# Optimization experiments

Measured on AMD Instinct MI355X. Metric: run time of the kernel, lower is better.

Reference implementation:

```python
import jax, jax.numpy as jnp
import numpy as np

N, T, D, M = 16, 4096, 256, 512


def setup_inputs() -> dict:
    key = jax.random.key(0)
    k1, k2 = jax.random.split(key)
    x = jax.random.normal(k1, (N, T, D), dtype=jnp.float32)
    # codebook initialized like the module: uniform(-1/M, 1/M) then row-normalized
    init_bound = 1.0 / M
    emb = jax.random.uniform(k2, (M, D), dtype=jnp.float32, minval=-init_bound, maxval=init_bound)
    emb = emb / (jnp.linalg.norm(emb, axis=1, keepdims=True) + 1e-4)
    return {"x": x, "embedding": emb}


def reference(x, embedding):
    sg = jax.lax.stop_gradient
    # L2_distance: distances computed against the row-normalized codebook,
    # but the gather uses the raw (unnormalized) codebook.
    emb_norm = embedding / (jnp.linalg.norm(embedding, axis=1, keepdims=True) + 1e-4)
    x_flat = sg(x).reshape(-1, D)  # (N*T, D), detached in torch
    distances = (jnp.sum(emb_norm ** 2, axis=1)[None, :]
                 + jnp.sum(x_flat ** 2, axis=1, keepdims=True)
                 - 2.0 * (x_flat @ emb_norm.T))  # (N*T, M)
    indices = jnp.argmin(distances, axis=-1)  # (N*T,)
    encodings = jax.nn.one_hot(indices, M, dtype=jnp.float32)  # (N*T, M)
    quantized = embedding[indices].reshape(x.shape)  # (N, T, D)

    commitment_loss = jnp.mean((sg(x) - quantized) ** 2)
    quantized_ = x + sg(quantized - x)           # straight-through
    quantized_ = (quantized_ + quantized) / 2.0  # averaged with raw-grad path

    avg_probs = jnp.mean(encodings, axis=0)  # (M,)
    perplexity = jnp.exp(-jnp.sum(avg_probs * jnp.log(avg_probs + 1e-10)))
    return quantized_, commitment_loss, perplexity
```

## Files before the change

### kernel.cpp

```cpp
#include <hip/hip_runtime.h>
#include <hip/hip_bf16.h>


typedef _Float16 half8_t __attribute__((ext_vector_type(8)));
typedef _Float16 half4_t __attribute__((ext_vector_type(4)));
typedef float f32x4 __attribute__((ext_vector_type(4)));

static constexpr int kRows = 65536;
static constexpr int kD = 256;
static constexpr int kM = 512;

typedef const unsigned int __attribute__((address_space(1)))* gas_t;
typedef unsigned int __attribute__((address_space(3)))* las_t;

__global__ void vq_prep(const float* __restrict__ emb, _Float16* __restrict__ swz,
                        float* __restrict__ bias, unsigned int* __restrict__ hist,
                        float* __restrict__ loss) {
    const int j = blockIdx.x;
    const int lane = threadIdx.x;
    float4 v = ((const float4*)(emb + j * kD))[lane];
    float ss = v.x * v.x + v.y * v.y + v.z * v.z + v.w * v.w;
    #pragma unroll
    for (int off = 32; off > 0; off >>= 1) ss += __shfl_xor(ss, off);
    const float scale = 1.0f / (sqrtf(ss) + 1e-4f);
    if (lane == 0) bias[j] = 0.5f * ss * scale * scale;
    half4_t h;
    h[0] = (_Float16)(v.x * scale);
    h[1] = (_Float16)(v.y * scale);
    h[2] = (_Float16)(v.z * scale);
    h[3] = (_Float16)(v.w * scale);
    const int k0 = lane * 4;
    const int ko = k0 >> 5;
    const int qd = (k0 >> 3) & 3;
    const int jj = k0 & 7;
    const int off_h = (j >> 4) * 4096 + ko * 512 + (qd * 16 + (j & 15)) * 8 + jj;
    *(half4_t*)(swz + off_h) = h;
    if (j == 0) {
        for (int b = lane; b < kM; b += 64) hist[b] = 0u;
        if (lane == 0) loss[0] = 0.0f;
    }
}

__global__ __launch_bounds__(128, 2) void vq_argmin(
    const float* __restrict__ x, const _Float16* __restrict__ bswz,
    const float* __restrict__ bias, unsigned int* __restrict__ hist,
    int* __restrict__ idx_out) {
    __shared__ _Float16 bb[2][32 * kD];
    __shared__ float lbias[kM];
    __shared__ unsigned int lhist[kM];

    const int t = threadIdx.x;
    const int row0 = blockIdx.x * 64;
    const int wave = t >> 6;
    const int lane = t & 63;
    const int qd = lane >> 4;
    const int ln = lane & 15;

    #pragma unroll
    for (int b = t; b < kM; b += 128) { lhist[b] = 0u; lbias[b] = bias[b]; }

    half8_t a[2][8];
    #pragma unroll
    for (int s = 0; s < 2; ++s) {
        const float* xr = x + (size_t)(row0 + wave * 32 + s * 16 + ln) * kD + qd * 8;
        #pragma unroll
        for (int ko = 0; ko < 8; ++ko) {
            const float4 v0 = *(const float4*)(xr + ko * 32);
            const float4 v1 = *(const float4*)(xr + ko * 32 + 4);
            half8_t h;
            h[0] = (_Float16)v0.x; h[1] = (_Float16)v0.y;
            h[2] = (_Float16)v0.z; h[3] = (_Float16)v0.w;
            h[4] = (_Float16)v1.x; h[5] = (_Float16)v1.y;
            h[6] = (_Float16)v1.z; h[7] = (_Float16)v1.w;
            a[s][ko] = h;
        }
    }

    auto stage_load = [&](int st, int buf) {
        const _Float16* src = bswz + (size_t)st * 8192 + t * 8;
        _Float16* dst = &bb[buf][0] + t * 8;
        #pragma unroll
        for (int i = 0; i < 8; ++i)
            __builtin_amdgcn_global_load_lds((gas_t)(const void*)(src + i * 1024),
                                             (las_t)(void*)(dst + i * 1024), 16, 0, 0);
    };

    stage_load(0, 0);

    float bv[2][4] = {{-1e30f, -1e30f, -1e30f, -1e30f}, {-1e30f, -1e30f, -1e30f, -1e30f}};
    int bi[2][4] = {{0, 0, 0, 0}, {0, 0, 0, 0}};
    #pragma unroll 1
    for (int st = 0; st < 16; ++st) {
        if (st < 15) stage_load(st + 1, (st + 1) & 1);
        if (st == 0)       __asm__ __volatile__("s_waitcnt vmcnt(8) lgkmcnt(0)\ns_barrier" ::: "memory");
        else if (st < 15)  __asm__ __volatile__("s_waitcnt vmcnt(8)\ns_barrier" ::: "memory");
        else               __asm__ __volatile__("s_waitcnt vmcnt(0)\ns_barrier" ::: "memory");

        const _Float16* bbase = &bb[st & 1][0];
        #pragma unroll
        for (int sg = 0; sg < 2; ++sg) {
            const int c = st * 32 + sg * 16 + ln;
            const float bbias = lbias[c];
            f32x4 acc0 = {-bbias, -bbias, -bbias, -bbias};
            f32x4 acc1 = {-bbias, -bbias, -bbias, -bbias};
            const half8_t* bp = (const half8_t*)bbase + sg * 512 + lane;
            #pragma unroll
            for (int ko = 0; ko < 8; ++ko) {
                const half8_t bf = bp[ko * 64];
                acc0 = __builtin_amdgcn_mfma_f32_16x16x32_f16(a[0][ko], bf, acc0, 0, 0, 0);
                acc1 = __builtin_amdgcn_mfma_f32_16x16x32_f16(a[1][ko], bf, acc1, 0, 0, 0);
            }
            #pragma unroll
            for (int r = 0; r < 4; ++r) {
                if (acc0[r] > bv[0][r]) { bv[0][r] = acc0[r]; bi[0][r] = c; }
                if (acc1[r] > bv[1][r]) { bv[1][r] = acc1[r]; bi[1][r] = c; }
            }
        }
        if (st < 15) __asm__ __volatile__("s_barrier" ::: "memory");
    }

    #pragma unroll
    for (int s = 0; s < 2; ++s) {
        #pragma unroll
        for (int r = 0; r < 4; ++r) {
            #pragma unroll
            for (int off = 1; off < 16; off <<= 1) {
                const float ov = __shfl_xor(bv[s][r], off);
                const int oi = __shfl_xor(bi[s][r], off);
                if (ov > bv[s][r] || (ov == bv[s][r] && oi < bi[s][r])) { bv[s][r] = ov; bi[s][r] = oi; }
            }
            if (ln == 0) {
                idx_out[row0 + wave * 32 + s * 16 + qd * 4 + r] = bi[s][r];
                atomicAdd(&lhist[bi[s][r]], 1u);
            }
        }
    }
    __syncthreads();

    #pragma unroll
    for (int b = t; b < kM; b += 128) {
        const unsigned int h = lhist[b];
        if (h) atomicAdd(&hist[b], h);
    }
}

__global__ __launch_bounds__(256) void vq_epilogue(
    const float* __restrict__ x, const float* __restrict__ emb,
    const int* __restrict__ idx, float* __restrict__ loss_accum,
    float* __restrict__ out) {
    __shared__ int li[64];
    __shared__ float lred[4];
    const int t = threadIdx.x;
    const int row0 = blockIdx.x * 64;
    if (t < 64) li[t] = idx[row0 + t];
    __syncthreads();

    float lsum = 0.0f;
    const float* xg = x + (size_t)row0 * kD;
    float* og = out + (size_t)row0 * kD;
    #pragma unroll
    for (int i = 0; i < 16; ++i) {
        const int g = t * 4 + i * 1024;
        const int r = g >> 8;
        const float4 xv = *(const float4*)(xg + g);
        const float4 q = *(const float4*)(emb + (size_t)li[r] * kD + (g & 255));
        const float d0 = xv.x - q.x, d1 = xv.y - q.y, d2 = xv.z - q.z, d3 = xv.w - q.w;
        lsum += d0 * d0 + d1 * d1 + d2 * d2 + d3 * d3;
        float4 o;
        o.x = ((xv.x + (q.x - xv.x)) + q.x) * 0.5f;
        o.y = ((xv.y + (q.y - xv.y)) + q.y) * 0.5f;
        o.z = ((xv.z + (q.z - xv.z)) + q.z) * 0.5f;
        o.w = ((xv.w + (q.w - xv.w)) + q.w) * 0.5f;
        *(float4*)&og[g] = o;
    }
    #pragma unroll
    for (int off = 32; off > 0; off >>= 1) lsum += __shfl_xor(lsum, off);
    if ((t & 63) == 0) lred[t >> 6] = lsum;
    __syncthreads();
    if (t == 0) atomicAdd(loss_accum, lred[0] + lred[1] + lred[2] + lred[3]);
}

__global__ void vq_final(const unsigned int* __restrict__ hist,
                         const float* __restrict__ loss_accum,
                         float* __restrict__ out) {
    const int t = threadIdx.x;
    __shared__ float sr[4];
    float s = 0.0f;
    for (int b = t; b < kM; b += 256) {
        const float p = (float)hist[b] * (1.0f / 65536.0f);
        s += p * logf(p + 1e-10f);
    }
    #pragma unroll
    for (int off = 32; off > 0; off >>= 1) s += __shfl_xor(s, off);
    if ((t & 63) == 0) sr[t >> 6] = s;
    __syncthreads();
    if (t == 0) {
        const float tot = sr[0] + sr[1] + sr[2] + sr[3];
        out[16777217] = expf(-tot);
        out[16777216] = loss_accum[0] * (1.0f / 16777216.0f);
    }
}

extern "C" void kernel_launch(void* const* d_in, const int* in_sizes, int n_in,
                              void* d_out, int out_size, void* d_ws, size_t ws_size,
                              hipStream_t stream) {
    const float* x = (const float*)d_in[0];
    const float* emb = (const float*)d_in[1];
    char* ws = (char*)d_ws;
    _Float16* bswz = (_Float16*)ws;
    float* bias = (float*)(ws + 262144);
    unsigned int* hist = (unsigned int*)(ws + 262144 + 2048);
    float* loss = (float*)(ws + 262144 + 4096);
    int* idx = (int*)(ws + 262144 + 4096 + 64);
    float* out = (float*)d_out;

    vq_prep<<<kM, 64, 0, stream>>>(emb, bswz, bias, hist, loss);
    vq_argmin<<<kRows / 64, 128, 0, stream>>>(x, bswz, bias, hist, idx);
    vq_epilogue<<<kRows / 64, 256, 0, stream>>>(x, emb, idx, loss, out);
    vq_final<<<1, 256, 0, stream>>>(hist, loss, out);
}
```

Measured before the change: 167.4 us.

## Keep codebook fragments in registers and stage x tile in LDS for argmin

Restructures the argmin kernel so each of 8 waves holds a 64-code slice of the fp16 codebook in registers, while a 128-row x tile is converted to fp16 and stored in padded LDS. Scores are offset by 64 so they stay positive, then packed with the code index into a uint so that argmax becomes an integer max. Per-wave winners are reduced across waves through shared memory. This removes the per-stage codebook streaming and barriers, at the cost of heavy register use (64 half8 B fragments) and precision lost by truncating low mantissa bits, which may change tie-breaking on near-equal distances.

```diff
diff --git a/kernel.cpp b/kernel.cpp
--- a/kernel.cpp
+++ b/kernel.cpp
@@ -9,9 +9,7 @@
 static constexpr int kRows = 65536;
 static constexpr int kD = 256;
 static constexpr int kM = 512;
-
-typedef const unsigned int __attribute__((address_space(1)))* gas_t;
-typedef unsigned int __attribute__((address_space(3)))* las_t;
+static constexpr int kSH = 264;
 
 __global__ void vq_prep(const float* __restrict__ emb, _Float16* __restrict__ swz,
                         float* __restrict__ bias, unsigned int* __restrict__ hist,
@@ -41,106 +39,106 @@
     }
 }
 
-__global__ __launch_bounds__(128, 2) void vq_argmin(
+__global__ __launch_bounds__(512, 2) void vq_argmin(
     const float* __restrict__ x, const _Float16* __restrict__ bswz,
     const float* __restrict__ bias, unsigned int* __restrict__ hist,
     int* __restrict__ idx_out) {
-    __shared__ _Float16 bb[2][32 * kD];
-    __shared__ float lbias[kM];
+    __shared__ _Float16 xs[2][64 * kSH];
+    __shared__ unsigned int red[8 * 128];
     __shared__ unsigned int lhist[kM];
 
     const int t = threadIdx.x;
-    const int row0 = blockIdx.x * 64;
+    const int row0 = blockIdx.x * 128;
     const int wave = t >> 6;
     const int lane = t & 63;
     const int qd = lane >> 4;
     const int ln = lane & 15;
 
-    #pragma unroll
-    for (int b = t; b < kM; b += 128) { lhist[b] = 0u; lbias[b] = bias[b]; }
-
-    half8_t a[2][8];
-    #pragma unroll
-    for (int s = 0; s < 2; ++s) {
-        const float* xr = x + (size_t)(row0 + wave * 32 + s * 16 + ln) * kD + qd * 8;
-        #pragma unroll
-        for (int ko = 0; ko < 8; ++ko) {
-            const float4 v0 = *(const float4*)(xr + ko * 32);
-            const float4 v1 = *(const float4*)(xr + ko * 32 + 4);
+    lhist[t] = 0u;
+
+    half8_t bfrag[4][8];
+    #pragma unroll
+    for (int nt = 0; nt < 4; ++nt)
+        #pragma unroll
+        for (int ko = 0; ko < 8; ++ko)
+            bfrag[nt][ko] = *(const half8_t*)(bswz + (size_t)(wave * 4 + nt) * 4096 + ko * 512 + lane * 8);
+
+    float binit[4];
+    #pragma unroll
+    for (int nt = 0; nt < 4; ++nt) binit[nt] = 64.0f - bias[wave * 64 + nt * 16 + ln];
+
+    {
+        const float* xg = x + (size_t)row0 * kD;
+        #pragma unroll
+        for (int i = 0; i < 8; ++i) {
+            const int fi = t * 8 + i * 4096;
+            const float4 v0 = *(const float4*)(xg + fi);
+            const float4 v1 = *(const float4*)(xg + fi + 4);
+            const int r = fi >> 8, c = fi & 255;
             half8_t h;
             h[0] = (_Float16)v0.x; h[1] = (_Float16)v0.y;
             h[2] = (_Float16)v0.z; h[3] = (_Float16)v0.w;
             h[4] = (_Float16)v1.x; h[5] = (_Float16)v1.y;
             h[6] = (_Float16)v1.z; h[7] = (_Float16)v1.w;
-            a[s][ko] = h;
+            *(half8_t*)&xs[r >> 6][(r & 63) * kSH + c] = h;
         }
     }
-
-    auto stage_load = [&](int st, int buf) {
-        const _Float16* src = bswz + (size_t)st * 8192 + t * 8;
-        _Float16* dst = &bb[buf][0] + t * 8;
-        #pragma unroll
-        for (int i = 0; i < 8; ++i)
-            __builtin_amdgcn_global_load_lds((gas_t)(const void*)(src + i * 1024),
-                                             (las_t)(void*)(dst + i * 1024), 16, 0, 0);
-    };
-
-    stage_load(0, 0);
-
-    float bv[2][4] = {{-1e30f, -1e30f, -1e30f, -1e30f}, {-1e30f, -1e30f, -1e30f, -1e30f}};
-    int bi[2][4] = {{0, 0, 0, 0}, {0, 0, 0, 0}};
+    __syncthreads();
+
     #pragma unroll 1
-    for (int st = 0; st < 16; ++st) {
-        if (st < 15) stage_load(st + 1, (st + 1) & 1);
-        if (st == 0)       __asm__ __volatile__("s_waitcnt vmcnt(8) lgkmcnt(0)\ns_barrier" ::: "memory");
-        else if (st < 15)  __asm__ __volatile__("s_waitcnt vmcnt(8)\ns_barrier" ::: "memory");
-        else               __asm__ __volatile__("s_waitcnt vmcnt(0)\ns_barrier" ::: "memory");
-
-        const _Float16* bbase = &bb[st & 1][0];
-        #pragma unroll
-        for (int sg = 0; sg < 2; ++sg) {
-            const int c = st * 32 + sg * 16 + ln;
-            const float bbias = lbias[c];
-            f32x4 acc0 = {-bbias, -bbias, -bbias, -bbias};
-            f32x4 acc1 = {-bbias, -bbias, -bbias, -bbias};
-            const half8_t* bp = (const half8_t*)bbase + sg * 512 + lane;
+    for (int tile = 0; tile < 2; ++tile) {
+        const _Float16* xb = &xs[tile][0];
+        #pragma unroll
+        for (int mt = 0; mt < 4; ++mt) {
+            half8_t a[8];
             #pragma unroll
-            for (int ko = 0; ko < 8; ++ko) {
-                const half8_t bf = bp[ko * 64];
-                acc0 = __builtin_amdgcn_mfma_f32_16x16x32_f16(a[0][ko], bf, acc0, 0, 0, 0);
-                acc1 = __builtin_amdgcn_mfma_f32_16x16x32_f16(a[1][ko], bf, acc1, 0, 0, 0);
+            for (int ko = 0; ko < 8; ++ko)
+                a[ko] = *(const half8_t*)(xb + (mt * 16 + ln) * kSH + qd * 8 + ko * 32);
+            unsigned int best[4] = {0u, 0u, 0u, 0u};
+            #pragma unroll
+            for (int nt = 0; nt < 4; ++nt) {
+                f32x4 acc = {binit[nt], binit[nt], binit[nt], binit[nt]};
+                #pragma unroll
+                for (int ko = 0; ko < 8; ++ko)
+                    acc = __builtin_amdgcn_mfma_f32_16x16x32_f16(a[ko], bfrag[nt][ko], acc, 0, 0, 0);
+                const unsigned int code = wave * 64 + nt * 16 + ln;
+                #pragma unroll
+                for (int r = 0; r < 4; ++r) {
+                    const unsigned int pk = (__float_as_uint(acc[r]) & 0xFFFFFE00u) | code;
+                    best[r] = best[r] > pk ? best[r] : pk;
+                }
             }
             #pragma unroll
-            for (int r = 0; r < 4; ++r) {
-                if (acc0[r] > bv[0][r]) { bv[0][r] = acc0[r]; bi[0][r] = c; }
-                if (acc1[r] > bv[1][r]) { bv[1][r] = acc1[r]; bi[1][r] = c; }
+            for (int off = 1; off < 16; off <<= 1) {
+                #pragma unroll
+                for (int r = 0; r < 4; ++r) {
+                    const unsigned int o = (unsigned int)__shfl_xor((int)best[r], off);
+                    best[r] = best[r] > o ? best[r] : o;
+                }
+            }
+            if (ln == 0) {
+                uint4 v; v.x = best[0]; v.y = best[1]; v.z = best[2]; v.w = best[3];
+                *(uint4*)&red[wave * 128 + tile * 64 + mt * 16 + qd * 4] = v;
             }
         }
-        if (st < 15) __asm__ __volatile__("s_barrier" ::: "memory");
-    }
-
-    #pragma unroll
-    for (int s = 0; s < 2; ++s) {
-        #pragma unroll
-        for (int r = 0; r < 4; ++r) {
-            #pragma unroll
-            for (int off = 1; off < 16; off <<= 1) {
-                const float ov = __shfl_xor(bv[s][r], off);
-                const int oi = __shfl_xor(bi[s][r], off);
-                if (ov > bv[s][r] || (ov == bv[s][r] && oi < bi[s][r])) { bv[s][r] = ov; bi[s][r] = oi; }
-            }
-            if (ln == 0) {
-                idx_out[row0 + wave * 32 + s * 16 + qd * 4 + r] = bi[s][r];
-                atomicAdd(&lhist[bi[s][r]], 1u);
-            }
+    }
+    __syncthreads();
+
+    if (t < 128) {
+        unsigned int m = red[t];
+        #pragma unroll
+        for (int w = 1; w < 8; ++w) {
+            const unsigned int o = red[w * 128 + t];
+            m = m > o ? m : o;
         }
-    }
-    __syncthreads();
-
-    #pragma unroll
-    for (int b = t; b < kM; b += 128) {
-        const unsigned int h = lhist[b];
-        if (h) atomicAdd(&hist[b], h);
+        const int idx = (int)(m & 511u);
+        idx_out[row0 + t] = idx;
+        atomicAdd(&lhist[idx], 1u);
+    }
+    __syncthreads();
+    {
+        const unsigned int h = lhist[t];
+        if (h) atomicAdd(&hist[t], h);
     }
 }
 
@@ -215,7 +213,7 @@
     float* out = (float*)d_out;
 
     vq_prep<<<kM, 64, 0, stream>>>(emb, bswz, bias, hist, loss);
-    vq_argmin<<<kRows / 64, 128, 0, stream>>>(x, bswz, bias, hist, idx);
+    vq_argmin<<<kRows / 128, 512, 0, stream>>>(x, bswz, bias, hist, idx);
     vq_epilogue<<<kRows / 64, 256, 0, stream>>>(x, emb, idx, loss, out);
     vq_final<<<1, 256, 0, stream>>>(hist, loss, out);
 }
```

Result: faster. 152.9 us (-8.7%).
